# Optimization experiments

Measured on AMD Instinct MI355X. Metric: run time of the kernel, lower is better.

Reference implementation:

```python
import jax, jax.numpy as jnp
import numpy as np

N_LAYERS = 11
DILATIONS = tuple(2 ** i for i in range(N_LAYERS))   # 1..1024
MEM_SIZES = DILATIONS                                 # kernel=2 -> 1 past tap -> mem = dilation
HOP = 128
C_SCALE = 1.0
FFT = 256       # channel width
NUM_CLS = 256   # mu-law classes
COND = 80       # mel bands
FRAMES = 16


def setup_inputs() -> dict:
    key = jax.random.key(0)
    ks = jax.random.split(key, 10)
    s = 0.05  # keep logits well-scaled for softmax sampling
    return {
        "y": jax.random.normal(ks[0], (COND, FRAMES), jnp.float32),
        "samples": jax.random.uniform(ks[1], (FRAMES * HOP,), jnp.float32),
        "emb_raw": jax.random.normal(ks[2], (NUM_CLS, FFT), jnp.float32) * 0.5,
        "condition_W": jax.random.normal(ks[3], (N_LAYERS * FFT, COND), jnp.float32) * s,
        "WV_past": jax.random.normal(ks[4], (N_LAYERS, FFT, FFT, 1), jnp.float32) * s,
        "WV_present": jax.random.normal(ks[5], (N_LAYERS, FFT, FFT), jnp.float32) * s,
        "W_o_w": jax.random.normal(ks[6], (N_LAYERS, FFT, FFT), jnp.float32) * s,
        "W_o_b": jax.random.normal(ks[7], (N_LAYERS, FFT), jnp.float32) * s,
        "end_w": jax.random.normal(ks[8], (NUM_CLS, FFT), jnp.float32) * s,
        "end_b": jax.random.normal(ks[9], (NUM_CLS,), jnp.float32) * s,
    }


def reference(y, samples, emb_raw, condition_W, WV_past, WV_present, W_o_w, W_o_b, end_w, end_b):
    emb = jnp.tanh(emb_raw)                      # fftnet.emb[0].weight.tanh()
    T = y.shape[1] * HOP
    # F.interpolate nearest with scale_factor=hop_length == frame repeat
    yu = jnp.repeat(y, HOP, axis=1)              # [COND, T]
    # precompute all conditioning projections (condition_W @ y[:, i], chunked per layer)
    conds = (condition_W @ yu).reshape(N_LAYERS, FFT, T).transpose(2, 0, 1)  # [T, L, FFT]

    bufs0 = tuple(jnp.zeros((FFT, m), jnp.float32) for m in MEM_SIZES)
    x0 = emb[NUM_CLS // 2 - 1]
    n_taps = WV_past.shape[3]

    def step(carry, inp):
        x, bufs = carry
        cond_t, u, t = inp
        new_bufs = []
        for j in range(N_LAYERS):
            mem = bufs[j]
            m = MEM_SIZES[j]
            idx = t % m                                   # ring-buffer write/oldest-read ptr
            h = cond_t[j]
            ii = idx
            for k in range(n_taps):                       # read past taps (before write)
                h = h + WV_past[j, :, :, k] @ mem[:, ii]
                ii = (ii + DILATIONS[j]) % m
            h = h + WV_present[j] @ x
            new_bufs.append(mem.at[:, idx].set(x))        # write current x into ring buffer
            h = jax.nn.relu(h)
            z = W_o_w[j] @ h + W_o_b[j]
            x = jax.nn.relu(z + x)                        # residual + relu
        logits = (end_w @ x + end_b) * C_SCALE
        cum = jnp.cumsum(jax.nn.softmax(logits))
        new_idx = jnp.argmax(cum > u)                     # nonzero(cum > u)[0]
        return (emb[new_idx], tuple(new_bufs)), new_idx

    ts = jnp.arange(T)
    _, outputs = jax.lax.scan(step, (x0, bufs0), (conds, samples, ts))
    return outputs  # [T] int sampled mu-law classes
```

## Files before the change

### kernel.cpp

```cpp
#include <hip/hip_runtime.h>
#include <math.h>


#define T_STEPS 2048
#define NBLK    53

typedef unsigned long long u64;
typedef float v64f __attribute__((ext_vector_type(64)));

#define OFF_EMBT   0
#define OFF_WPET   65536
#define OFF_WVPET  131072
#define OFF_RINGS  196608
#define OFF_TAPQ   1244672
#define OFF_ZQ4    1408512
#define OFF_XQ     1431040
#define OFF_IDXQ   1436672
#define WS_FLOATS  1436736

#define FBAR(r)  (32*(r))

__device__ __forceinline__ float ldc(const float* p) {
  int v = __hip_atomic_load((const int*)p, __ATOMIC_RELAXED, __HIP_MEMORY_SCOPE_AGENT);
  return __int_as_float(v);
}
__device__ __forceinline__ void stc(float* p, float x) {
  __hip_atomic_store((int*)p, __float_as_int(x), __ATOMIC_RELAXED, __HIP_MEMORY_SCOPE_AGENT);
}
__device__ __forceinline__ u64 ldq(const u64* p) {
  return __hip_atomic_load(p, __ATOMIC_RELAXED, __HIP_MEMORY_SCOPE_AGENT);
}
__device__ __forceinline__ void stq(u64* p, float v, int tag) {
  u64 x = (u64)(unsigned)__float_as_int(v) | ((u64)(unsigned)tag << 32);
  __hip_atomic_store(p, x, __ATOMIC_RELAXED, __HIP_MEMORY_SCOPE_AGENT);
}
__device__ __forceinline__ int ptag(u64 q) { return (int)(q >> 32); }
__device__ __forceinline__ float pval(u64 q) { return __int_as_float((int)(unsigned)q); }

__device__ __forceinline__ float spin_pair(const u64* p, int want) {
  int bud = 1 << 20; u64 q;
  do { q = ldq(p); } while (ptag(q) < want && --bud > 0);
  return pval(q);
}
__device__ __forceinline__ int spin_idx(const u64* p, int want) {
  int bud = 1 << 20; u64 q;
  do { q = ldq(p); } while (ptag(q) < want && --bud > 0);
  return __float_as_int(pval(q)) & 255;
}
__device__ __forceinline__ void spin2(const u64* p1, const u64* p2, int want,
                                      float& v1, float& v2) {
  int bud = 1 << 20; u64 q1, q2; bool ok;
  do {
    q1 = ldq(p1); q2 = ldq(p2);
    ok = (ptag(q1) >= want) & (ptag(q2) >= want);
  } while (!ok && --bud > 0);
  v1 = pval(q1); v2 = pval(q2);
}
__device__ __forceinline__ void spin5(const u64* p0, const u64* p1, const u64* p2,
                                      const u64* p3, const u64* p4, int want,
                                      float& v0, float& v1, float& v2, float& v3, float& v4) {
  int bud = 1 << 20; u64 q0, q1, q2, q3, q4; bool ok;
  do {
    q0 = ldq(p0); q1 = ldq(p1); q2 = ldq(p2); q3 = ldq(p3); q4 = ldq(p4);
    ok = (ptag(q0) >= want) & (ptag(q1) >= want) & (ptag(q2) >= want)
       & (ptag(q3) >= want) & (ptag(q4) >= want);
  } while (!ok && --bud > 0);
  v0 = pval(q0); v1 = pval(q1); v2 = pval(q2); v3 = pval(q3); v4 = pval(q4);
}
__device__ __forceinline__ void spin_tag2(const u64* p1, const u64* p2, int w1, int w2) {
  int bud = 1 << 20; u64 q1, q2; bool ok;
  do {
    q1 = ldq(p1); q2 = ldq(p2);
    ok = (ptag(q1) >= w1) & (ptag(q2) >= w2);
  } while (!ok && --bud > 0);
}
__device__ __forceinline__ void wait1(int* f, int want) {
  int it = 0;
  while (__hip_atomic_load(f, __ATOMIC_RELAXED, __HIP_MEMORY_SCOPE_AGENT) < want) {
    if (++it > (1 << 22)) break;
  }
  (void)__hip_atomic_load(f, __ATOMIC_ACQUIRE, __HIP_MEMORY_SCOPE_AGENT);
}
__device__ __forceinline__ void post(int* f, int v) {
  __hip_atomic_store(f, v, __ATOMIC_RELEASE, __HIP_MEMORY_SCOPE_AGENT);
}

__global__ __launch_bounds__(512, 1)
void fftnet_kernel(const float* __restrict__ y, const float* __restrict__ samples,
                   const float* __restrict__ emb_raw, const float* __restrict__ condW,
                   const float* __restrict__ WV_past, const float* __restrict__ WV_present,
                   const float* __restrict__ W_o_w, const float* __restrict__ W_o_b,
                   const float* __restrict__ end_w, const float* __restrict__ end_b,
                   int* __restrict__ out, float* __restrict__ ws)
{
  const int tid = threadIdx.x;
  const int bid = blockIdx.x;
  int* iflags = (int*)(ws + WS_FLOATS);
  u64* zq4  = (u64*)(ws + OFF_ZQ4);
  u64* xq   = (u64*)(ws + OFF_XQ);
  u64* tq   = (u64*)(ws + OFF_TAPQ);
  u64* idxq = (u64*)(ws + OFF_IDXQ);

  __shared__ float s_x[256];
  __shared__ float s_h[256];
  __shared__ float s_p[1024];
  __shared__ float s_cond[2048];
  __shared__ float s_tap[64];
  __shared__ float s_m[320];
  __shared__ unsigned long long s_mask[8];

  for (int i = bid * 512 + tid; i < 65536; i += NBLK * 512)
    stc(ws + OFF_EMBT + i, tanhf(emb_raw[i]));
  __syncthreads();
  if (tid == 0) post(iflags + FBAR(bid), 1);
  if (tid < NBLK) wait1(iflags + FBAR(tid), 1);
  __syncthreads();

  for (int n = bid; n < 512; n += NBLK) {
    const float* wmat = (n < 256) ? WV_present : WV_past;
    int cls = n & 255;
    int c = tid & 255, s2 = tid >> 8;
    float acc = 0.f;
    for (int k = 128 * s2; k < 128 * s2 + 128; ++k)
      acc += wmat[c * 256 + k] * ws[OFF_EMBT + cls * 256 + k];
    s_p[s2 * 256 + c] = acc;
    __syncthreads();
    if (tid < 256)
      stc(ws + ((n < 256) ? OFF_WPET : OFF_WVPET) + cls * 256 + tid, s_p[tid] + s_p[256 + tid]);
    __syncthreads();
  }
  __syncthreads();
  if (tid == 0) post(iflags + FBAR(bid), 2);
  if (tid < NBLK) wait1(iflags + FBAR(tid), 2);
  __syncthreads();
  __builtin_amdgcn_fence(__ATOMIC_ACQUIRE, "agent");
  __syncthreads();

  if (bid == 0) {
    const int c = tid & 255, s2 = tid >> 8;
    v64f we0;
#pragma unroll
    for (int i = 0; i < 64; ++i) we0[i] = end_w[c * 256 + 128 * s2 + i];
    const float eb = end_b[c];
    const float b10 = W_o_b[10 * 256 + c];
    const u64* pz0 = zq4 + (10 * 4 + 0) * 256;
    const u64* pz1 = zq4 + (10 * 4 + 1) * 256;
    const u64* pz2 = zq4 + (10 * 4 + 2) * 256;
    const u64* pz3 = zq4 + (10 * 4 + 3) * 256;
    const u64* pxq = xq + 10 * 256;
    const int lane = tid & 63, w = tid >> 6;
    if (tid == 0) stq(idxq, __int_as_float(127), 1);

    for (int t = 0; t < T_STEPS; ++t) {
      float u = samples[t];
      const float* ewp = end_w + c * 256 + 128 * s2 + 64;
      asm volatile("" : "+v"(ewp));
      ewp = (const float*)__builtin_assume_aligned(ewp, 16);
      v64f we1;
#pragma unroll
      for (int i = 0; i < 64; ++i) we1[i] = ewp[i];
      __builtin_amdgcn_sched_barrier(0);

      if (tid < 256) {
        float a, b, cc, d, r3;
        spin5(pz0 + tid, pz1 + tid, pz2 + tid, pz3 + tid, pxq + tid, t + 1, a, b, cc, d, r3);
        float s01 = a + b, s23 = cc + d;
        s_x[tid] = fmaxf(s01 + s23 + b10 + r3, 0.f);
      }
      __syncthreads();
      float acc = 0.f;
#pragma unroll
      for (int i = 0; i < 64; ++i) acc += we0[i] * s_x[128 * s2 + i];
#pragma unroll
      for (int i = 0; i < 64; ++i) acc += we1[i] * s_x[128 * s2 + 64 + i];
      s_p[s2 * 256 + c] = acc;
      __syncthreads();
      float logit = 0.f;
      if (tid < 256) logit = s_p[tid] + s_p[256 + tid] + eb;
      float vmax = (tid < 256) ? logit : -3.4e38f;
#pragma unroll
      for (int d2 = 32; d2 > 0; d2 >>= 1) vmax = fmaxf(vmax, __shfl_xor(vmax, d2, 64));
      if (lane == 0) s_m[280 + w] = vmax;
      __syncthreads();
      float mx = fmaxf(fmaxf(s_m[280], s_m[281]), fmaxf(s_m[282], s_m[283]));
      float e = (tid < 256) ? expf(logit - mx) : 0.f;
      float vs = e;
#pragma unroll
      for (int d2 = 32; d2 > 0; d2 >>= 1) vs += __shfl_xor(vs, d2, 64);
      if (lane == 0) s_m[288 + w] = vs;
      __syncthreads();
      float ssum = s_m[288] + s_m[289] + s_m[290] + s_m[291];
      float p = (tid < 256) ? (e / ssum) : 0.f;
      float v = p;
#pragma unroll
      for (int d2 = 1; d2 < 64; d2 <<= 1) {
        float o = __shfl_up(v, (unsigned)d2, 64);
        if (lane >= d2) v += o;
      }
      if (tid < 256 && lane == 63) s_m[256 + w] = v;
      __syncthreads();
      float offs = 0.f;
      if (tid < 256) for (int k = 0; k < w; ++k) offs += s_m[256 + k];
      float cum = v + offs;
      unsigned long long msk = __ballot(tid < 256 && (cum > u));
      if (lane == 0) s_mask[w] = msk;
      __syncthreads();
      if (tid == 0) {
        int idx = 0;
        for (int k = 0; k < 4; ++k) {
          unsigned long long m2 = s_mask[k];
          if (m2) { idx = k * 64 + (int)__builtin_ctzll(m2); break; }
        }
        stq(idxq, __int_as_float(idx), t + 2);
        out[t] = idx;
      }
      __syncthreads();
    }

  } else if (bid <= 2) {
    const int side = bid - 1;
    const int row = tid & 255, chunk = tid >> 8;
    v64f wv;
#pragma unroll
    for (int i = 0; i < 64; ++i)
      wv[i] = W_o_w[row * 256 + side * 128 + chunk * 64 + i];
    for (int e = tid; e < 2048; e += 512) {
      int f = e >> 7, rr = e & 127;
      float a = 0.f;
      for (int q = 0; q < 80; ++q) a += condW[(side * 128 + rr) * 80 + q] * y[q * 16 + f];
      s_cond[f * 128 + rr] = a;
    }
    __syncthreads();
    u64* zout = zq4 + (0 * 4 + side) * 256;
    int pidx = 127;

    for (int t = 0; t < T_STEPS; ++t) {
      int idx = pidx;
      if (tid < 128) {
        float tapv = (t > 0) ? ws[OFF_WVPET + pidx * 256 + side * 128 + tid] : 0.f;
        idx = spin_idx(idxq, t + 1);
        float hv = s_cond[(t >> 7) * 128 + tid]
                 + ws[OFF_WPET + idx * 256 + side * 128 + tid] + tapv;
        s_h[tid] = fmaxf(hv, 0.f);
        if (tid == 0) s_m[300] = __int_as_float(idx);
      }
      __syncthreads();
      float acc = 0.f;
#pragma unroll
      for (int i = 0; i < 64; ++i) acc += wv[i] * s_h[64 * chunk + i];
      s_p[chunk * 256 + row] = acc;
      __syncthreads();
      if (tid < 256) stq(zout + tid, s_p[tid] + s_p[256 + tid], t + 1);
      pidx = (tid < 128) ? idx : __float_as_int(s_m[300]);
      __syncthreads();
    }

  } else if (bid <= 42) {
    const int jj = 1 + ((bid - 3) >> 2);
    const int k  = (bid - 3) & 3;
    v64f wv;
    if (tid < 256) {
      int r = tid & 63, s = tid >> 6;
#pragma unroll
      for (int i = 0; i < 64; ++i)
        wv[i] = WV_present[jj * 65536 + (64 * k + r) * 256 + 64 * s + i];
    } else {
      int row = tid - 256;
#pragma unroll
      for (int i = 0; i < 64; ++i)
        wv[i] = W_o_w[jj * 65536 + row * 256 + 64 * k + i];
    }
    const float bprev = W_o_b[(jj - 1) * 256 + (tid & 255)];
    for (int e = tid; e < 1024; e += 512) {
      int f = e >> 6, rr = e & 63;
      float a = 0.f;
      for (int q = 0; q < 80; ++q)
        a += condW[(jj * 256 + 64 * k + rr) * 80 + q] * y[q * 16 + f];
      s_cond[f * 64 + rr] = a;
    }
    __syncthreads();
    const int dj = 1 << jj, maskj = 2 * dj - 1;
    float* ringj = ws + OFF_RINGS + 512 * (dj - 1);
    const u64* pz0 = zq4 + ((jj - 1) * 4 + 0) * 256;
    const u64* pz1 = zq4 + ((jj - 1) * 4 + 1) * 256;
    const u64* pz2 = zq4 + ((jj - 1) * 4 + 2) * 256;
    const u64* pz3 = zq4 + ((jj - 1) * 4 + 3) * 256;
    const u64* pxp = xq + (jj - 1) * 256;
    u64* zout = zq4 + (jj * 4 + k) * 256;
    u64* xout = xq + jj * 256;
    const u64* ptap = tq + (jj - 1) * 32 * 256;

    for (int t = 0; t < T_STEPS; ++t) {
      const int want = t + 1;
      if (tid < 256) {
        float xv;
        if (jj == 1) {
          int idx = spin_idx(idxq, want);
          float ev = ws[OFF_EMBT + idx * 256 + tid];
          float a, b;
          spin2(pz0 + tid, pz1 + tid, want, a, b);
          xv = fmaxf((a + b) + bprev + ev, 0.f);
        } else {
          float a, b, cc, d, xp;
          spin5(pz0 + tid, pz1 + tid, pz2 + tid, pz3 + tid, pxp + tid, want, a, b, cc, d, xp);
          float s01 = a + b, s23 = cc + d;
          xv = fmaxf(s01 + s23 + bprev + xp, 0.f);
        }
        s_x[tid] = xv;
        if (k == 0) stq(xout + tid, xv, want);
      } else if (tid >= 384 && tid < 448) {
        int l = tid - 384;
        s_tap[l] = spin_pair(ptap + (t & 31) * 256 + 64 * k + l, want);
      }
      __syncthreads();
      if (tid < 256) {
        int r = tid & 63, s = tid >> 6;
        float acc = 0.f;
#pragma unroll
        for (int i = 0; i < 64; ++i) acc += wv[i] * s_x[64 * s + i];
        s_p[s * 64 + r] = acc;
      } else if (k == 0) {
        int row = tid - 256;
        stc(ringj + (t & maskj) * 256 + row, s_x[row]);
      }
      __syncthreads();
      if (tid < 64) {
        float hv = s_p[tid] + s_p[64 + tid] + s_p[128 + tid] + s_p[192 + tid]
                 + s_cond[(t >> 7) * 64 + tid] + s_tap[tid];
        s_h[tid] = fmaxf(hv, 0.f);
      }
      __syncthreads();
      if (tid >= 256) {
        int row = tid - 256;
        float acc = 0.f;
#pragma unroll
        for (int i = 0; i < 64; ++i) acc += wv[i] * s_h[i];
        if (k == 0)
          __builtin_amdgcn_fence(__ATOMIC_RELEASE, "agent");
        stq(zout + row, acc, want);
      }
      __syncthreads();
    }

  } else {
    const int j = bid - 42;
    const int dj = 1 << j, maskj = 2 * dj - 1;
    v64f wq0, wq1;
    { int r = tid & 255, s2 = tid >> 8;
#pragma unroll
      for (int i = 0; i < 64; ++i) wq0[i] = WV_past[j * 65536 + r * 256 + 128 * s2 + i];
#pragma unroll
      for (int i = 0; i < 64; ++i) wq1[i] = WV_past[j * 65536 + r * 256 + 128 * s2 + 64 + i]; }
    float* ringj = ws + OFF_RINGS + 512 * (dj - 1);
    u64* tapj = tq + (j - 1) * 32 * 256;
    const u64* z0 = zq4 + (j * 4 + 0) * 256;

    for (int t = 0; t < T_STEPS; ++t) {
      int g0 = t - 31;
      if (t >= dj && t - dj + 1 > g0) g0 = t - dj + 1;
      int gk = t - 31;
      if (tid < 256 && (g0 >= 1 || gk >= 1)) {
        const u64* zk = zq4 + (j * 4 + (tid >> 6)) * 256;
        spin_tag2(z0 + tid, zk + tid, g0, gk);
      }
      float tapv = 0.f;
      if (t >= dj) {
        if (tid < 256) s_x[tid] = ldc(ringj + ((t - dj) & maskj) * 256 + tid);
        __syncthreads();
        int r = tid & 255, s2 = tid >> 8;
        float acc = 0.f;
#pragma unroll
        for (int i = 0; i < 64; ++i) acc += wq0[i] * s_x[128 * s2 + i];
#pragma unroll
        for (int i = 0; i < 64; ++i) acc += wq1[i] * s_x[128 * s2 + 64 + i];
        s_p[s2 * 256 + r] = acc;
        __syncthreads();
        if (tid < 256) tapv = s_p[tid] + s_p[256 + tid];
      }
      if (tid < 256) stq(tapj + (t & 31) * 256 + tid, tapv, t + 1);
      __syncthreads();
    }
  }
}

extern "C" void kernel_launch(void* const* d_in, const int* in_sizes, int n_in,
                              void* d_out, int out_size, void* d_ws, size_t ws_size,
                              hipStream_t stream) {
  const float* y       = (const float*)d_in[0];
  const float* samples = (const float*)d_in[1];
  const float* emb_raw = (const float*)d_in[2];
  const float* condW   = (const float*)d_in[3];
  const float* WV_past = (const float*)d_in[4];
  const float* WV_pres = (const float*)d_in[5];
  const float* W_o_w   = (const float*)d_in[6];
  const float* W_o_b   = (const float*)d_in[7];
  const float* end_w   = (const float*)d_in[8];
  const float* end_b   = (const float*)d_in[9];
  (void)in_sizes; (void)n_in; (void)out_size; (void)ws_size;
  hipLaunchKernelGGL(fftnet_kernel, dim3(NBLK), dim3(512), 0, stream,
                     y, samples, emb_raw, condW, WV_past, WV_pres,
                     W_o_w, W_o_b, end_w, end_b, (int*)d_out, (float*)d_ws);
}
```

Baseline: 50.94 ms.

## Add adaptive pre-sleep before spin waits and reduce partial sums via shuffles

Spinning waves in the producer and consumer blocks now sleep for an adaptively tuned number of s_sleep intervals before polling. The count is adjusted each step from how many polls the previous wait needed, with the aim of cutting memory-polling contention. Row/chunk thread mappings are reordered so partial dot-product sums are combined with wave shuffles instead of an LDS round trip, which removes one __syncthreads per step in the layer and first-layer blocks. spin_tag2 gains a short sleep and a smaller budget. The risk is extra latency on the serial critical path if the sleeps overshoot.

New measurement: 51.70 ms. No clear change (+1.5%).

```diff
diff --git a/kernel.cpp b/kernel.cpp
--- a/kernel.cpp
+++ b/kernel.cpp
@@ -37,6 +37,17 @@
 __device__ __forceinline__ int ptag(u64 q) { return (int)(q >> 32); }
 __device__ __forceinline__ float pval(u64 q) { return __int_as_float((int)(unsigned)q); }
 
+__device__ __forceinline__ void presleep_n(int n) {
+  for (int i = 0; i < n; ++i) __builtin_amdgcn_s_sleep(127);
+}
+__device__ __forceinline__ int adapt_u(int uu, int it, int t) {
+  if (t >= 2) {
+    if (it <= 1 && uu > 0) --uu;
+    else if (it >= 8 && uu < 6) ++uu;
+  }
+  return uu;
+}
+
 __device__ __forceinline__ float spin_pair(const u64* p, int want) {
   int bud = 1 << 20; u64 q;
   do { q = ldq(p); } while (ptag(q) < want && --bud > 0);
@@ -47,31 +58,38 @@
   do { q = ldq(p); } while (ptag(q) < want && --bud > 0);
   return __float_as_int(pval(q)) & 255;
 }
-__device__ __forceinline__ void spin2(const u64* p1, const u64* p2, int want,
-                                      float& v1, float& v2) {
-  int bud = 1 << 20; u64 q1, q2; bool ok;
+__device__ __forceinline__ int spin_idxc(const u64* p, int want, int& it) {
+  int bud = 1 << 20; u64 q; it = 0;
+  do { q = ldq(p); ++it; } while (ptag(q) < want && --bud > 0);
+  return __float_as_int(pval(q)) & 255;
+}
+__device__ __forceinline__ void spin2c(const u64* p1, const u64* p2, int want,
+                                       float& v1, float& v2, int& it) {
+  int bud = 1 << 20; u64 q1, q2; bool ok; it = 0;
   do {
-    q1 = ldq(p1); q2 = ldq(p2);
+    q1 = ldq(p1); q2 = ldq(p2); ++it;
     ok = (ptag(q1) >= want) & (ptag(q2) >= want);
   } while (!ok && --bud > 0);
   v1 = pval(q1); v2 = pval(q2);
 }
-__device__ __forceinline__ void spin5(const u64* p0, const u64* p1, const u64* p2,
-                                      const u64* p3, const u64* p4, int want,
-                                      float& v0, float& v1, float& v2, float& v3, float& v4) {
-  int bud = 1 << 20; u64 q0, q1, q2, q3, q4; bool ok;
+__device__ __forceinline__ void spin5c(const u64* p0, const u64* p1, const u64* p2,
+                                       const u64* p3, const u64* p4, int want,
+                                       float& v0, float& v1, float& v2, float& v3,
+                                       float& v4, int& it) {
+  int bud = 1 << 20; u64 q0, q1, q2, q3, q4; bool ok; it = 0;
   do {
-    q0 = ldq(p0); q1 = ldq(p1); q2 = ldq(p2); q3 = ldq(p3); q4 = ldq(p4);
+    q0 = ldq(p0); q1 = ldq(p1); q2 = ldq(p2); q3 = ldq(p3); q4 = ldq(p4); ++it;
     ok = (ptag(q0) >= want) & (ptag(q1) >= want) & (ptag(q2) >= want)
        & (ptag(q3) >= want) & (ptag(q4) >= want);
   } while (!ok && --bud > 0);
   v0 = pval(q0); v1 = pval(q1); v2 = pval(q2); v3 = pval(q3); v4 = pval(q4);
 }
 __device__ __forceinline__ void spin_tag2(const u64* p1, const u64* p2, int w1, int w2) {
-  int bud = 1 << 20; u64 q1, q2; bool ok;
+  int bud = 1 << 18; u64 q1, q2; bool ok;
   do {
     q1 = ldq(p1); q2 = ldq(p2);
     ok = (ptag(q1) >= w1) & (ptag(q2) >= w2);
+    if (!ok) __builtin_amdgcn_s_sleep(31);
   } while (!ok && --bud > 0);
 }
 __device__ __forceinline__ void wait1(int* f, int want) {
@@ -149,7 +167,8 @@
     const u64* pz3 = zq4 + (10 * 4 + 3) * 256;
     const u64* pxq = xq + 10 * 256;
     const int lane = tid & 63, w = tid >> 6;
-    if (tid == 0) stq(idxq, __int_as_float(127), 1);
+    if (tid == 0) { stq(idxq, __int_as_float(127), 1); s_m[301] = __int_as_float(3); }
+    __syncthreads();
 
     for (int t = 0; t < T_STEPS; ++t) {
       float u = samples[t];
@@ -162,8 +181,12 @@
       __builtin_amdgcn_sched_barrier(0);
 
       if (tid < 256) {
-        float a, b, cc, d, r3;
-        spin5(pz0 + tid, pz1 + tid, pz2 + tid, pz3 + tid, pxq + tid, t + 1, a, b, cc, d, r3);
+        int uu = __float_as_int(s_m[301]);
+        if (t >= 2) presleep_n(uu);
+        float a, b, cc, d, r3; int it;
+        spin5c(pz0 + tid, pz1 + tid, pz2 + tid, pz3 + tid, pxq + tid, t + 1,
+               a, b, cc, d, r3, it);
+        if (tid == 0) s_m[301] = __int_as_float(adapt_u(uu, it, t));
         float s01 = a + b, s23 = cc + d;
         s_x[tid] = fmaxf(s01 + s23 + b10 + r3, 0.f);
       }
@@ -219,7 +242,7 @@
 
   } else if (bid <= 2) {
     const int side = bid - 1;
-    const int row = tid & 255, chunk = tid >> 8;
+    const int row = tid >> 1, chunk = tid & 1;
     v64f wv;
 #pragma unroll
     for (int i = 0; i < 64; ++i)
@@ -230,28 +253,33 @@
       for (int q = 0; q < 80; ++q) a += condW[(side * 128 + rr) * 80 + q] * y[q * 16 + f];
       s_cond[f * 128 + rr] = a;
     }
+    if (tid == 0) s_m[301] = __int_as_float(3);
     __syncthreads();
     u64* zout = zq4 + (0 * 4 + side) * 256;
     int pidx = 127;
 
     for (int t = 0; t < T_STEPS; ++t) {
-      int idx = pidx;
       if (tid < 128) {
         float tapv = (t > 0) ? ws[OFF_WVPET + pidx * 256 + side * 128 + tid] : 0.f;
-        idx = spin_idx(idxq, t + 1);
+        int uu = __float_as_int(s_m[301]);
+        if (t >= 2) presleep_n(uu);
+        int it;
+        int idx = spin_idxc(idxq, t + 1, it);
+        if (tid == 0) s_m[301] = __int_as_float(adapt_u(uu, it, t));
         float hv = s_cond[(t >> 7) * 128 + tid]
                  + ws[OFF_WPET + idx * 256 + side * 128 + tid] + tapv;
         s_h[tid] = fmaxf(hv, 0.f);
-        if (tid == 0) s_m[300] = __int_as_float(idx);
+        pidx = idx;
       }
       __syncthreads();
       float acc = 0.f;
 #pragma unroll
       for (int i = 0; i < 64; ++i) acc += wv[i] * s_h[64 * chunk + i];
-      s_p[chunk * 256 + row] = acc;
-      __syncthreads();
-      if (tid < 256) stq(zout + tid, s_p[tid] + s_p[256 + tid], t + 1);
-      pidx = (tid < 128) ? idx : __float_as_int(s_m[300]);
+      {
+        int lb = (tid & 63) & ~1;
+        float o = __shfl(acc, lb + 1, 64);
+        if (chunk == 0) stq(zout + row, acc + o, t + 1);
+      }
       __syncthreads();
     }
 
@@ -260,7 +288,7 @@
     const int k  = (bid - 3) & 3;
     v64f wv;
     if (tid < 256) {
-      int r = tid & 63, s = tid >> 6;
+      int r = tid >> 2, s = tid & 3;
 #pragma unroll
       for (int i = 0; i < 64; ++i)
         wv[i] = WV_present[jj * 65536 + (64 * k + r) * 256 + 64 * s + i];
@@ -278,6 +306,7 @@
         a += condW[(jj * 256 + 64 * k + rr) * 80 + q] * y[q * 16 + f];
       s_cond[f * 64 + rr] = a;
     }
+    if (tid == 0) s_m[301] = __int_as_float(3);
     __syncthreads();
     const int dj = 1 << jj, maskj = 2 * dj - 1;
     float* ringj = ws + OFF_RINGS + 512 * (dj - 1);
@@ -294,18 +323,23 @@
       const int want = t + 1;
       if (tid < 256) {
         float xv;
+        int uu = __float_as_int(s_m[301]);
+        if (t >= 2) presleep_n(uu);
+        int it;
         if (jj == 1) {
           int idx = spin_idx(idxq, want);
           float ev = ws[OFF_EMBT + idx * 256 + tid];
           float a, b;
-          spin2(pz0 + tid, pz1 + tid, want, a, b);
+          spin2c(pz0 + tid, pz1 + tid, want, a, b, it);
           xv = fmaxf((a + b) + bprev + ev, 0.f);
         } else {
           float a, b, cc, d, xp;
-          spin5(pz0 + tid, pz1 + tid, pz2 + tid, pz3 + tid, pxp + tid, want, a, b, cc, d, xp);
+          spin5c(pz0 + tid, pz1 + tid, pz2 + tid, pz3 + tid, pxp + tid, want,
+                 a, b, cc, d, xp, it);
           float s01 = a + b, s23 = cc + d;
           xv = fmaxf(s01 + s23 + bprev + xp, 0.f);
         }
+        if (tid == 0) s_m[301] = __int_as_float(adapt_u(uu, it, t));
         s_x[tid] = xv;
         if (k == 0) stq(xout + tid, xv, want);
       } else if (tid >= 384 && tid < 448) {
@@ -314,20 +348,22 @@
       }
       __syncthreads();
       if (tid < 256) {
-        int r = tid & 63, s = tid >> 6;
+        int r = tid >> 2, s = tid & 3;
         float acc = 0.f;
 #pragma unroll
         for (int i = 0; i < 64; ++i) acc += wv[i] * s_x[64 * s + i];
-        s_p[s * 64 + r] = acc;
+        int lb = (tid & 63) & ~3;
+        float p1 = __shfl(acc, lb + 1, 64);
+        float p2 = __shfl(acc, lb + 2, 64);
+        float p3 = __shfl(acc, lb + 3, 64);
+        if (s == 0) {
+          float hv = ((acc + p1) + p2) + p3
+                   + s_cond[(t >> 7) * 64 + r] + s_tap[r];
+          s_h[r] = fmaxf(hv, 0.f);
+        }
       } else if (k == 0) {
         int row = tid - 256;
         stc(ringj + (t & maskj) * 256 + row, s_x[row]);
-      }
-      __syncthreads();
-      if (tid < 64) {
-        float hv = s_p[tid] + s_p[64 + tid] + s_p[128 + tid] + s_p[192 + tid]
-                 + s_cond[(t >> 7) * 64 + tid] + s_tap[tid];
-        s_h[tid] = fmaxf(hv, 0.f);
       }
       __syncthreads();
       if (tid >= 256) {
```
